# Kernel optimization log

Hardware: AMD Instinct MI355X
Metric: run time of the kernel (lower is better)

## Reference

```python
import jax, jax.numpy as jnp
import numpy as np


def setup_inputs() -> dict:
    key = jax.random.key(0)
    k0, k1, k2, k3, k4, k5 = jax.random.split(key, 6)
    B, H, P, L = 8, 128, 128, 4096
    u = jax.random.normal(k0, (B, H, L), dtype=jnp.float32)
    C2 = jax.random.normal(k1, (H, P, 2), dtype=jnp.float32)        # view_as_real(C)
    B_bar2 = jax.random.normal(k2, (P, H, 2), dtype=jnp.float32)    # view_as_real(B_bar)
    D = jax.random.normal(k3, (H, H), dtype=jnp.float32)
    # Frozen discrete diagonal state matrix: |lambda| in [strong, weak] = [0.9, 1.0]
    r = 0.9 + 0.1 * jax.random.uniform(k4, (P,), dtype=jnp.float32)
    th = 2.0 * jnp.pi * jax.random.uniform(k5, (P,), dtype=jnp.float32)
    Lambda_bar2 = jnp.stack([r * jnp.cos(th), r * jnp.sin(th)], axis=-1)
    return {"u": u, "C2": C2, "B_bar2": B_bar2, "D": D, "Lambda_bar2": Lambda_bar2}


def reference(u, C2, B_bar2, D, Lambda_bar2):
    L = u.shape[-1]
    Lam = Lambda_bar2[:, 0] + 1j * Lambda_bar2[:, 1]           # (P,)
    omega = 2.0 * jnp.pi * jnp.fft.rfftfreq(L).astype(jnp.float32)  # (Lf,)
    # Cauchy-like frequency kernel: 1 / (i*omega - Lambda)  -> (P, Lf)
    kernel = 1.0 / (1j * omega[None, :] - Lam[:, None])
    C = C2[..., 0] + 1j * C2[..., 1]                           # (H, P)
    B_bar = B_bar2[..., 0] + 1j * B_bar2[..., 1]               # (P, H)
    U_s = jnp.fft.rfftn(u)                                     # n-dim FFT (faithful to torch.fft.rfftn(u))
    C_kernel = jnp.einsum('hp,pl->hpl', C, kernel)             # (H, P, Lf)
    G = jnp.einsum('hpl,pq->hql', C_kernel, B_bar)             # (H, H, Lf)
    Y_s = jnp.einsum('hql,bql->bhl', G, U_s) + jnp.einsum('hq,bql->bhl', D.astype(U_s.dtype), U_s)
    y = jnp.fft.irfftn(Y_s)                                    # (B, H, L)
    return jax.nn.gelu(y, approximate=False)                   # torch nn.GELU default = exact erf
```

## Files before the change

### kernel.cpp

```cpp
#include <hip/hip_runtime.h>
#include <math.h>

#define PI_F 3.14159265358979323846f
#define NB 8
#define NH 128
#define NL 4096
#define LF 2049
#define WB 2064
#define NT 16512

typedef float2 cpx;
typedef __attribute__((ext_vector_type(8))) short bf8v;
typedef __attribute__((ext_vector_type(4))) float f4;

#define MFMA16(a, b, c) __builtin_amdgcn_mfma_f32_16x16x32_bf16(a, b, c, 0, 0, 0)

__device__ __forceinline__ float gelu_exact(float x) {
  return 0.5f * x * (1.0f + erff(x * 0.70710678118654752f));
}
__device__ __forceinline__ unsigned short f2bf(float f) {
  unsigned int x = __float_as_uint(f);
  return (unsigned short)((x + 0x7FFFu + ((x >> 16) & 1u)) >> 16);
}
__device__ __forceinline__ float bf2f(unsigned short h) {
  return __uint_as_float((unsigned int)h << 16);
}
__device__ __forceinline__ unsigned int packpair(float re, float im) {
  return (unsigned int)f2bf(re) | ((unsigned int)f2bf(im) << 16);
}
__device__ __forceinline__ cpx cadd(cpx a, cpx b) { return make_float2(a.x + b.x, a.y + b.y); }
__device__ __forceinline__ cpx csub(cpx a, cpx b) { return make_float2(a.x - b.x, a.y - b.y); }
__device__ __forceinline__ cpx cmul(cpx a, cpx b) {
  return make_float2(fmaf(a.x, b.x, -a.y * b.y), fmaf(a.x, b.y, a.y * b.x));
}
template <int SGN>
__device__ __forceinline__ cpx mulJ(cpx a) {
  return (SGN < 0) ? make_float2(a.y, -a.x) : make_float2(-a.y, a.x);
}

__global__ __launch_bounds__(128) void precomp_pack(
    const float* __restrict__ C2, const float* __restrict__ B2,
    const float* __restrict__ D,
    unsigned short* __restrict__ Mbh, unsigned short* __restrict__ Mbl,
    unsigned short* __restrict__ Mch, unsigned short* __restrict__ Mcl) {
  __shared__ float rc[128], rs[128];
  __shared__ float sTr[128], sTi[128];
  int x = blockIdx.x, t = threadIdx.x, which = blockIdx.y;
  { float s, c; sincosf(-(2.f * PI_F / 128.f) * (float)t, &s, &c); rc[t] = c; rs[t] = s; }
  __syncthreads();
  float sr = 0.f, si = 0.f;
  if (which == 0) {
    for (int k = 0; k < 128; ++k) {
      int j = (k * t) & 127; float c = rc[j], s = rs[j];
      float br = B2[(x * 128 + k) * 2], bi = B2[(x * 128 + k) * 2 + 1];
      sr += br * c - bi * s; si += br * s + bi * c;
    }
    auto wr = [&](int r, int c, float v) {
      unsigned short h = f2bf(v);
      Mbh[r * 256 + c] = h; Mbl[r * 256 + c] = f2bf(v - bf2f(h));
    };
    wr(2 * x,     2 * t,     sr);  wr(2 * x,     2 * t + 1, -si);
    wr(2 * x + 1, 2 * t,     si);  wr(2 * x + 1, 2 * t + 1,  sr);
  } else if (which == 1) {
    for (int k = 0; k < 128; ++k) {
      int j = (k * t) & 127; float c = rc[j], s = -rs[j];
      float cr = C2[(k * 128 + x) * 2], ci = C2[(k * 128 + x) * 2 + 1];
      sr += cr * c - ci * s; si += cr * s + ci * c;
    }
    sr *= (1.f / 128.f); si *= (1.f / 128.f);
    auto wr = [&](int r, int c, float v) {
      unsigned short h = f2bf(v);
      Mch[r * 512 + c] = h; Mcl[r * 512 + c] = f2bf(v - bf2f(h));
    };
    wr(2 * t,     2 * x,     sr);  wr(2 * t,     2 * x + 1, -si);
    wr(2 * t + 1, 2 * x,     si);  wr(2 * t + 1, 2 * x + 1,  sr);
  } else {
    for (int k = 0; k < 128; ++k) {
      int j = (k * x) & 127; float c = rc[j], s = rs[j];
      float d = D[t * 128 + k];
      sr += d * c; si += d * s;
    }
    sTr[t] = sr; sTi[t] = si;
    __syncthreads();
    sr = 0.f; si = 0.f;
    for (int k = 0; k < 128; ++k) {
      int j = (k * t) & 127; float c = rc[j], s = -rs[j];
      sr += sTr[k] * c - sTi[k] * s;
      si += sTr[k] * s + sTi[k] * c;
    }
    sr *= (1.f / 128.f); si *= (1.f / 128.f);
    auto wr = [&](int r, int c, float v) {
      unsigned short h = f2bf(v);
      Mch[r * 512 + c] = h; Mcl[r * 512 + c] = f2bf(v - bf2f(h));
    };
    wr(2 * t,     256 + 2 * x,     sr);  wr(2 * t,     256 + 2 * x + 1, -si);
    wr(2 * t + 1, 256 + 2 * x,     si);  wr(2 * t + 1, 256 + 2 * x + 1,  sr);
  }
}

#define SW(k) ((k) ^ (((k) >> 4) & 31))

template <int SGN>
__device__ __forceinline__ void dft8(cpx a[8]) {
  cpx t0 = cadd(a[0], a[4]), u0 = csub(a[0], a[4]);
  cpx t1 = cadd(a[1], a[5]), u1 = csub(a[1], a[5]);
  cpx t2 = cadd(a[2], a[6]), u2 = csub(a[2], a[6]);
  cpx t3 = cadd(a[3], a[7]), u3 = csub(a[3], a[7]);
  cpx E0 = cadd(t0, t2), E2 = csub(t0, t2);
  cpx ju2 = mulJ<SGN>(u2);
  cpx E1 = cadd(u0, ju2), E3 = csub(u0, ju2);
  cpx O0 = cadd(t1, t3), O2 = csub(t1, t3);
  cpx ju3 = mulJ<SGN>(u3);
  cpx O1 = cadd(u1, ju3), O3 = csub(u1, ju3);
  const float r = 0.70710678118654752f;
  const float S = (float)SGN;
  cpx w1O1 = make_float2(r * (O1.x - S * O1.y), r * (O1.y + S * O1.x));
  cpx w3O3 = make_float2(r * (-O3.x - S * O3.y), r * (S * O3.x - O3.y));
  cpx jO2 = mulJ<SGN>(O2);
  a[0] = cadd(E0, O0);   a[4] = csub(E0, O0);
  a[1] = cadd(E1, w1O1); a[5] = csub(E1, w1O1);
  a[2] = cadd(E2, jO2);  a[6] = csub(E2, jO2);
  a[3] = cadd(E3, w3O3); a[7] = csub(E3, w3O3);
}

template <int SGN>
__device__ __forceinline__ void dft4(cpx b[4]) {
  cpx s0 = cadd(b[0], b[2]), d0 = csub(b[0], b[2]);
  cpx s1 = cadd(b[1], b[3]), d1 = csub(b[1], b[3]);
  cpx jd1 = mulJ<SGN>(d1);
  b[0] = cadd(s0, s1); b[2] = csub(s0, s1);
  b[1] = cadd(d0, jd1); b[3] = csub(d0, jd1);
}

__device__ __forceinline__ void twid8(cpx a[8], float ang) {
  float s, c; __sincosf(ang, &s, &c);
  cpx w1 = make_float2(c, s);
  cpx w2 = cmul(w1, w1), w3 = cmul(w2, w1), w4 = cmul(w2, w2);
  cpx w5 = cmul(w3, w2), w6 = cmul(w3, w3), w7 = cmul(w4, w3);
  a[1] = cmul(a[1], w1); a[2] = cmul(a[2], w2); a[3] = cmul(a[3], w3);
  a[4] = cmul(a[4], w4); a[5] = cmul(a[5], w5); a[6] = cmul(a[6], w6);
  a[7] = cmul(a[7], w7);
}

template <int SGN>
__device__ __forceinline__ void fft2048_core(cpx a[8], cpx* __restrict__ bufA,
                                             cpx* __restrict__ bufB, int t) {
  const float S = (float)SGN;
  dft8<SGN>(a);
  twid8(a, S * (2.f * PI_F / 2048.f) * (float)t);
#pragma unroll
  for (int p = 0; p < 8; ++p) bufA[p * 264 + t] = a[p];
  __syncthreads();
  int p = t >> 5, n1 = t & 31;
#pragma unroll
  for (int j = 0; j < 8; ++j) a[j] = bufA[p * 264 + n1 + 32 * j];
  dft8<SGN>(a);
  twid8(a, S * (2.f * PI_F / 256.f) * (float)n1);
#pragma unroll
  for (int q = 0; q < 8; ++q) bufB[p * 264 + q * 33 + n1] = a[q];
  __syncthreads();
  int q = (t >> 2) & 7, n2 = t & 3;
#pragma unroll
  for (int j = 0; j < 8; ++j) a[j] = bufB[p * 264 + q * 33 + n2 + 4 * j];
  dft8<SGN>(a);
  twid8(a, S * (2.f * PI_F / 32.f) * (float)n2);
#pragma unroll
  for (int d = 0; d < 8; ++d) bufA[p * 264 + q * 33 + 4 * d + n2] = a[d];
  __syncthreads();
#pragma unroll
  for (int h = 0; h < 2; ++h) {
    int d = 2 * n2 + h;
    cpx b[4];
#pragma unroll
    for (int m = 0; m < 4; ++m) b[m] = bufA[p * 264 + q * 33 + 4 * d + m];
    dft4<SGN>(b);
    int kb = p + 8 * q + 64 * d;
#pragma unroll
    for (int c = 0; c < 4; ++c) bufB[SW(kb + 512 * c)] = b[c];
  }
  __syncthreads();
}

__global__ __launch_bounds__(256) void fft_fwd_pack(const float* __restrict__ u,
                                                    unsigned int* __restrict__ Uph) {
  __shared__ cpx bufA[2112], bufB[2112];
  int t = threadIdx.x;
  int row = blockIdx.x;
  int b = row >> 7, q = row & 127;
  const cpx* src = (const cpx*)(u + (size_t)row * NL);
  cpx a[8];
#pragma unroll
  for (int j = 0; j < 8; ++j) a[j] = src[t + 256 * j];
  fft2048_core<-1>(a, bufA, bufB, t);
  unsigned int* Uh = Uph + (size_t)q * NT + (size_t)b * WB;
  auto pstore = [&](int k, float ur, float ui) { Uh[k] = packpair(ur, ui); };
#pragma unroll
  for (int r = 0; r < 4; ++r) {
    int k = t + (r << 8);
    if (k == 0) {
      cpx z0 = bufB[SW(0)];
      pstore(0, z0.x + z0.y, 0.f);
      pstore(2048, z0.x - z0.y, 0.f);
      cpx zN = bufB[SW(1024)];
      pstore(1024, zN.x, -zN.y);
    } else {
      cpx A = bufB[SW(k)];
      cpx M = bufB[SW(2048 - k)];
      float Br = M.x, Bi = -M.y;
      float sr = 0.5f * (A.x + Br), si = 0.5f * (A.y + Bi);
      float dr = 0.5f * (A.x - Br), di = 0.5f * (A.y - Bi);
      float th = (float)k * (PI_F / 2048.f);
      float sn, cs; __sincosf(th, &sn, &cs);
      float tr = cs * dr + sn * di;
      float ti = cs * di - sn * dr;
      pstore(k, sr + ti, si - tr);
      float A2r = M.x, A2i = M.y;
      float B2r = A.x, B2i = -A.y;
      float s2r = 0.5f * (A2r + B2r), s2i = 0.5f * (A2i + B2i);
      float d2r = 0.5f * (A2r - B2r), d2i = 0.5f * (A2i - B2i);
      float t2r = -cs * d2r + sn * d2i;
      float t2i = -cs * d2i - sn * d2r;
      pstore(2048 - k, s2r + t2i, s2i - t2r);
    }
  }
}

__global__ __launch_bounds__(256, 2) void gemm_fused(
    const unsigned short* __restrict__ Mbh, const unsigned short* __restrict__ Mbl,
    const unsigned short* __restrict__ Mch, const unsigned short* __restrict__ Mcl,
    const unsigned int* __restrict__ Uph,
    const float* __restrict__ Lam,
    float2* __restrict__ Yp) {
  __shared__ unsigned short Ah[8192], Al[8192];
  __shared__ unsigned short Bh[2048];
  __shared__ unsigned int Vl[8192];
  int tid = threadIdx.x;
  int j0 = blockIdx.x * 64;
  int w = tid >> 6, lane = tid & 63, quad = lane >> 4, ln = lane & 15;
  int colB = tid & 63, grpB = tid >> 6;
  f4 acc[4][4];
#pragma unroll
  for (int mt = 0; mt < 4; ++mt)
#pragma unroll
    for (int nt = 0; nt < 4; ++nt) acc[mt][nt] = (f4){0.f, 0.f, 0.f, 0.f};

  for (int kt = 0; kt < 256; kt += 32) {
    __syncthreads();
#pragma unroll
    for (int r = 0; r < 4; ++r) {
      int j = tid + 256 * r; int m = j >> 2, cch = j & 3;
      int slot = (m * 4 + (cch ^ (m & 3))) * 8;
      size_t go = (size_t)m * 256 + kt + cch * 8;
      *(uint4*)&Ah[slot] = *(const uint4*)&Mbh[go];
      *(uint4*)&Al[slot] = *(const uint4*)&Mbl[go];
    }
    {
      size_t base = (size_t)((kt >> 1) + grpB * 4) * NT + j0 + colB;
      uint4 hv;
      hv.x = Uph[base];          hv.y = Uph[base + NT];
      hv.z = Uph[base + 2 * NT]; hv.w = Uph[base + 3 * NT];
      *(uint4*)&Bh[(grpB * 64 + colB) * 8] = hv;
    }
    __syncthreads();
    bf8v ah[4], al[4], bh[4];
#pragma unroll
    for (int mt = 0; mt < 4; ++mt) {
      int m = w * 64 + mt * 16 + ln;
      int off = (m * 4 + (quad ^ (m & 3))) * 8;
      ah[mt] = *(const bf8v*)&Ah[off];
      al[mt] = *(const bf8v*)&Al[off];
    }
#pragma unroll
    for (int nt = 0; nt < 4; ++nt)
      bh[nt] = *(const bf8v*)&Bh[(quad * 64 + nt * 16 + ln) * 8];
#pragma unroll
    for (int mt = 0; mt < 4; ++mt)
#pragma unroll
      for (int nt = 0; nt < 4; ++nt) {
        acc[mt][nt] = MFMA16(ah[mt], bh[nt], acc[mt][nt]);
        acc[mt][nt] = MFMA16(al[mt], bh[nt], acc[mt][nt]);
      }
  }
  __syncthreads();
#pragma unroll
  for (int mt = 0; mt < 4; ++mt) {
    int r0 = w * 64 + mt * 16 + quad * 4;
    int p0 = r0 >> 1;
    float2 lam0 = ((const float2*)Lam)[p0];
    float2 lam1 = ((const float2*)Lam)[p0 + 1];
#pragma unroll
    for (int nt = 0; nt < 4; ++nt) {
      int col = nt * 16 + ln;
      int gcol = j0 + col;
      int bb = gcol / WB; int l = gcol - bb * WB;
      float omega = (float)l * (PI_F / 2048.f);
      f4 a = acc[mt][nt];
      float dx0 = -lam0.x, dy0 = omega - lam0.y;
      float inv0 = 1.f / (dx0 * dx0 + dy0 * dy0);
      float kr0 = dx0 * inv0, ki0 = -dy0 * inv0;
      float v0r = kr0 * a[0] - ki0 * a[1];
      float v0i = kr0 * a[1] + ki0 * a[0];
      float dx1 = -lam1.x, dy1 = omega - lam1.y;
      float inv1 = 1.f / (dx1 * dx1 + dy1 * dy1);
      float kr1 = dx1 * inv1, ki1 = -dy1 * inv1;
      float v1r = kr1 * a[2] - ki1 * a[3];
      float v1i = kr1 * a[3] + ki1 * a[2];
      int gc = (p0 >> 2) * 64 + col;
      Vl[gc * 4 + (p0 & 3)] = packpair(v0r, v0i);
      Vl[gc * 4 + ((p0 + 1) & 3)] = packpair(v1r, v1i);
    }
  }
  __syncthreads();

#pragma unroll
  for (int mt = 0; mt < 4; ++mt)
#pragma unroll
    for (int nt = 0; nt < 4; ++nt) acc[mt][nt] = (f4){0.f, 0.f, 0.f, 0.f};
  const unsigned short* Vs = (const unsigned short*)Vl;
  for (int kt = 0; kt < 512; kt += 32) {
    __syncthreads();
#pragma unroll
    for (int r = 0; r < 4; ++r) {
      int j = tid + 256 * r; int m = j >> 2, cch = j & 3;
      int slot = (m * 4 + (cch ^ (m & 3))) * 8;
      size_t go = (size_t)m * 512 + kt + cch * 8;
      *(uint4*)&Ah[slot] = *(const uint4*)&Mch[go];
      *(uint4*)&Al[slot] = *(const uint4*)&Mcl[go];
    }
    if (kt >= 256) {
      size_t base = (size_t)(((kt - 256) >> 1) + grpB * 4) * NT + j0 + colB;
      uint4 hv;
      hv.x = Uph[base];          hv.y = Uph[base + NT];
      hv.z = Uph[base + 2 * NT]; hv.w = Uph[base + 3 * NT];
      *(uint4*)&Bh[(grpB * 64 + colB) * 8] = hv;
    }
    __syncthreads();
    bf8v ah[4], al[4], bh[4];
#pragma unroll
    for (int mt = 0; mt < 4; ++mt) {
      int m = w * 64 + mt * 16 + ln;
      int off = (m * 4 + (quad ^ (m & 3))) * 8;
      ah[mt] = *(const bf8v*)&Ah[off];
      al[mt] = *(const bf8v*)&Al[off];
    }
    if (kt < 256) {
#pragma unroll
      for (int nt = 0; nt < 4; ++nt)
        bh[nt] = *(const bf8v*)&Vs[(((kt >> 3) + quad) * 64 + nt * 16 + ln) * 8];
    } else {
#pragma unroll
      for (int nt = 0; nt < 4; ++nt)
        bh[nt] = *(const bf8v*)&Bh[(quad * 64 + nt * 16 + ln) * 8];
    }
#pragma unroll
    for (int mt = 0; mt < 4; ++mt)
#pragma unroll
      for (int nt = 0; nt < 4; ++nt) {
        acc[mt][nt] = MFMA16(ah[mt], bh[nt], acc[mt][nt]);
        acc[mt][nt] = MFMA16(al[mt], bh[nt], acc[mt][nt]);
      }
  }
#pragma unroll
  for (int mt = 0; mt < 4; ++mt) {
    int r0 = w * 64 + mt * 16 + quad * 4;
    int h0 = r0 >> 1;
#pragma unroll
    for (int nt = 0; nt < 4; ++nt) {
      int gcol = j0 + nt * 16 + ln;
      f4 a = acc[mt][nt];
      Yp[(size_t)h0 * NT + gcol] = make_float2(a[0], a[1]);
      Yp[(size_t)(h0 + 1) * NT + gcol] = make_float2(a[2], a[3]);
    }
  }
}

__global__ __launch_bounds__(256) void fft_inv_gelu_pl(const float2* __restrict__ Yp,
                                                       float* __restrict__ out) {
  __shared__ cpx bufA[2112], bufB[2112];
  int t = threadIdx.x;
  int row = blockIdx.x;
  int b = row >> 7, h = row & 127;
  const float2* Yrow = Yp + (size_t)h * NT + (size_t)b * WB;
#pragma unroll
  for (int r = 0; r < 4; ++r) {
    int k = t + (r << 8);
    if (k == 0) {
      float y0 = Yrow[0].x;
      float yN = Yrow[2048].x;
      bufB[SW(0)] = make_float2(0.5f * (y0 + yN), 0.5f * (y0 - yN));
      float2 z = Yrow[1024];
      bufB[SW(1024)] = make_float2(z.x, -z.y);
    } else {
      float2 A = Yrow[k];
      float2 M = Yrow[2048 - k];
      float Br = M.x, Bi = -M.y;
      float sr = 0.5f * (A.x + Br), si = 0.5f * (A.y + Bi);
      float dr = 0.5f * (A.x - Br), di = 0.5f * (A.y - Bi);
      float th = (float)k * (PI_F / 2048.f);
      float sn, cs; __sincosf(th, &sn, &cs);
      float e1 = cs * di + sn * dr;
      float e2 = cs * dr - sn * di;
      bufB[SW(k)] = make_float2(sr - e1, si + e2);
      bufB[SW(2048 - k)] = make_float2(sr + e1, -si + e2);
    }
  }
  __syncthreads();
  cpx a[8];
#pragma unroll
  for (int j = 0; j < 8; ++j) a[j] = bufB[SW(t + 256 * j)];
  fft2048_core<1>(a, bufA, bufB, t);
  float2* dst = (float2*)(out + (size_t)row * NL);
  const float sc = 1.f / 2048.f;
#pragma unroll
  for (int r = 0; r < 8; ++r) {
    int n = t + (r << 8);
    cpx z = bufB[SW(n)];
    dst[n] = make_float2(gelu_exact(z.x * sc), gelu_exact(z.y * sc));
  }
}

__global__ __launch_bounds__(128) void fb_precomp(
    const float* __restrict__ C2, const float* __restrict__ B2,
    const float* __restrict__ D,
    float* __restrict__ Bt, float* __restrict__ Ct, float* __restrict__ Dt) {
  __shared__ float rc[128], rs[128];
  __shared__ float sTr[128], sTi[128];
  int x = blockIdx.x, t = threadIdx.x, which = blockIdx.y;
  { float s, c; sincosf(-(2.f * PI_F / 128.f) * (float)t, &s, &c); rc[t] = c; rs[t] = s; }
  __syncthreads();
  float sr = 0.f, si = 0.f;
  if (which == 0) {
    for (int k = 0; k < 128; ++k) {
      int j = (k * t) & 127; float c = rc[j], s = rs[j];
      float br = B2[(x * 128 + k) * 2], bi = B2[(x * 128 + k) * 2 + 1];
      sr += br * c - bi * s; si += br * s + bi * c;
    }
    Bt[(t * 128 + x) * 2] = sr; Bt[(t * 128 + x) * 2 + 1] = si;
  } else if (which == 1) {
    for (int k = 0; k < 128; ++k) {
      int j = (k * t) & 127; float c = rc[j], s = -rs[j];
      float cr = C2[(k * 128 + x) * 2], ci = C2[(k * 128 + x) * 2 + 1];
      sr += cr * c - ci * s; si += cr * s + ci * c;
    }
    Ct[(x * 128 + t) * 2] = sr * (1.f / 128.f);
    Ct[(x * 128 + t) * 2 + 1] = si * (1.f / 128.f);
  } else {
    for (int k = 0; k < 128; ++k) {
      int j = (k * x) & 127; float c = rc[j], s = rs[j];
      float d = D[t * 128 + k];
      sr += d * c; si += d * s;
    }
    sTr[t] = sr; sTi[t] = si;
    __syncthreads();
    sr = 0.f; si = 0.f;
    for (int k = 0; k < 128; ++k) {
      int j = (k * t) & 127; float c = rc[j], s = -rs[j];
      sr += sTr[k] * c - sTi[k] * s;
      si += sTr[k] * s + sTi[k] * c;
    }
    Dt[(x * 128 + t) * 2] = sr * (1.f / 128.f);
    Dt[(x * 128 + t) * 2 + 1] = si * (1.f / 128.f);
  }
}

__global__ __launch_bounds__(256) void fb_fft_fwd(const float* __restrict__ u,
                                                  cpx* __restrict__ U) {
  __shared__ cpx bufA[2112], bufB[2112];
  int t = threadIdx.x;
  int row = blockIdx.x;
  const cpx* src = (const cpx*)(u + (size_t)row * NL);
  cpx a[8];
#pragma unroll
  for (int j = 0; j < 8; ++j) a[j] = src[t + 256 * j];
  fft2048_core<-1>(a, bufA, bufB, t);
  cpx* Urow = U + (size_t)row * LF;
#pragma unroll
  for (int r = 0; r < 4; ++r) {
    int k = t + (r << 8);
    if (k == 0) {
      cpx z0 = bufB[SW(0)];
      Urow[0] = make_float2(z0.x + z0.y, 0.f);
      Urow[2048] = make_float2(z0.x - z0.y, 0.f);
      cpx zN = bufB[SW(1024)];
      Urow[1024] = make_float2(zN.x, -zN.y);
    } else {
      cpx A = bufB[SW(k)];
      cpx M = bufB[SW(2048 - k)];
      float Br = M.x, Bi = -M.y;
      float sr = 0.5f * (A.x + Br), si = 0.5f * (A.y + Bi);
      float dr = 0.5f * (A.x - Br), di = 0.5f * (A.y - Bi);
      float th = (float)k * (PI_F / 2048.f);
      float sn, cs; __sincosf(th, &sn, &cs);
      float tr = cs * dr + sn * di;
      float ti = cs * di - sn * dr;
      Urow[k] = make_float2(sr + ti, si - tr);
      float A2r = M.x, A2i = M.y;
      float B2r = A.x, B2i = -A.y;
      float s2r = 0.5f * (A2r + B2r), s2i = 0.5f * (A2i + B2i);
      float d2r = 0.5f * (A2r - B2r), d2i = 0.5f * (A2i - B2i);
      float t2r = -cs * d2r + sn * d2i;
      float t2i = -cs * d2i - sn * d2r;
      Urow[2048 - k] = make_float2(s2r + t2i, s2i - t2r);
    }
  }
}

__device__ __forceinline__ void ld4(float4 d[4], const float4* __restrict__ p) {
#pragma unroll
  for (int kk = 0; kk < 4; ++kk) d[kk] = p[kk];
}
__device__ __forceinline__ void cmac4(const float4 m[4], float xr, float xi,
                                      float ar[8], float ai[8]) {
#pragma unroll
  for (int kk = 0; kk < 4; ++kk) {
    float4 v = m[kk];
    ar[2 * kk]     = fmaf(v.x, xr, fmaf(-v.y, xi, ar[2 * kk]));
    ai[2 * kk]     = fmaf(v.x, xi, fmaf( v.y, xr, ai[2 * kk]));
    ar[2 * kk + 1] = fmaf(v.z, xr, fmaf(-v.w, xi, ar[2 * kk + 1]));
    ai[2 * kk + 1] = fmaf(v.z, xi, fmaf( v.w, xr, ai[2 * kk + 1]));
  }
}

__global__ __launch_bounds__(256) void fb_mix(
    const cpx* __restrict__ U,
    const float* __restrict__ Bt, const float* __restrict__ Ct,
    const float* __restrict__ Dt, const float* __restrict__ Lam,
    cpx* __restrict__ Y) {
  __shared__ cpx sU[128][17], sV[128][17];
  int tid = threadIdx.x;
  int b = blockIdx.y;
  size_t ub = (size_t)b * NH * LF;
  if (blockIdx.x == 128) {
    int t = tid;
    if (t < 128) sU[t][0] = U[ub + (size_t)t * LF + 2048];
    __syncthreads();
    if (t < 128) {
      float ar = 0.f, ai = 0.f;
      for (int q = 0; q < 128; ++q) {
        float ur = sU[q][0].x, ui = sU[q][0].y;
        float br = Bt[(q * 128 + t) * 2], bi = Bt[(q * 128 + t) * 2 + 1];
        ar = fmaf(br, ur, fmaf(-bi, ui, ar));
        ai = fmaf(br, ui, fmaf(bi, ur, ai));
      }
      float a = Lam[2 * t], bb = Lam[2 * t + 1];
      float dx = -a, dy = PI_F - bb;
      float inv = 1.f / (dx * dx + dy * dy);
      float kr = dx * inv, ki = -dy * inv;
      sV[t][0] = make_float2(kr * ar - ki * ai, kr * ai + ki * ar);
    }
    __syncthreads();
    if (t < 128) {
      float ar = 0.f, ai = 0.f;
      for (int q = 0; q < 128; ++q) {
        float ur = sU[q][0].x, ui = sU[q][0].y;
        float vr = sV[q][0].x, vi = sV[q][0].y;
        float cr = Ct[(q * 128 + t) * 2], ci = Ct[(q * 128 + t) * 2 + 1];
        float dr = Dt[(q * 128 + t) * 2], di = Dt[(q * 128 + t) * 2 + 1];
        ar += cr * vr - ci * vi + dr * ur - di * ui;
        ai += cr * vi + ci * vr + dr * ui + di * ur;
      }
      Y[ub + (size_t)t * LF + 2048] = make_float2(ar, ai);
    }
    return;
  }
  int lane = tid & 15, g = tid >> 4;
  int l = blockIdx.x * 16 + lane;
#pragma unroll
  for (int rep = 0; rep < 8; ++rep) {
    int q = rep * 16 + g;
    sU[q][lane] = U[ub + (size_t)q * LF + l];
  }
  __syncthreads();
  float omega = (float)l * (PI_F / 2048.f);
  float ar[8], ai[8];
  {
#pragma unroll
    for (int k = 0; k < 8; ++k) { ar[k] = 0.f; ai[k] = 0.f; }
    const float4* base = (const float4*)Bt + g * 4;
    float4 e[4], o[4];
    ld4(e, base);
#pragma unroll 1
    for (int q = 0; q < 128; q += 2) {
      ld4(o, base + (q + 1) * 64);
      cpx u0 = sU[q][lane];
      cmac4(e, u0.x, u0.y, ar, ai);
      ld4(e, base + ((q + 2) & 127) * 64);
      cpx u1 = sU[q + 1][lane];
      cmac4(o, u1.x, u1.y, ar, ai);
    }
    int p0 = g * 8;
#pragma unroll
    for (int k = 0; k < 8; ++k) {
      int p = p0 + k;
      float a = Lam[2 * p], bb = Lam[2 * p + 1];
      float dx = -a, dy = omega - bb;
      float inv = 1.f / (dx * dx + dy * dy);
      float kr = dx * inv, ki = -dy * inv;
      sV[p][lane] = make_float2(kr * ar[k] - ki * ai[k], kr * ai[k] + ki * ar[k]);
    }
  }
  __syncthreads();
  {
#pragma unroll
    for (int k = 0; k < 8; ++k) { ar[k] = 0.f; ai[k] = 0.f; }
    const float4* base = (const float4*)Ct + g * 4;
    float4 e[4], o[4];
    ld4(e, base);
#pragma unroll 1
    for (int q = 0; q < 128; q += 2) {
      ld4(o, base + (q + 1) * 64);
      cpx v0 = sV[q][lane];
      cmac4(e, v0.x, v0.y, ar, ai);
      ld4(e, base + ((q + 2) & 127) * 64);
      cpx v1 = sV[q + 1][lane];
      cmac4(o, v1.x, v1.y, ar, ai);
    }
  }
  {
    const float4* base = (const float4*)Dt + g * 4;
    float4 e[4], o[4];
    ld4(e, base);
#pragma unroll 1
    for (int q = 0; q < 128; q += 2) {
      ld4(o, base + (q + 1) * 64);
      cpx u0 = sU[q][lane];
      cmac4(e, u0.x, u0.y, ar, ai);
      ld4(e, base + ((q + 2) & 127) * 64);
      cpx u1 = sU[q + 1][lane];
      cmac4(o, u1.x, u1.y, ar, ai);
    }
  }
  int h0 = g * 8;
#pragma unroll
  for (int k = 0; k < 8; ++k) {
    Y[ub + (size_t)(h0 + k) * LF + l] = make_float2(ar[k], ai[k]);
  }
}

__global__ __launch_bounds__(256) void fb_fft_inv(const cpx* __restrict__ Y,
                                                  float* __restrict__ out) {
  __shared__ cpx bufA[2112], bufB[2112];
  int t = threadIdx.x;
  int row = blockIdx.x;
  const cpx* Yrow = Y + (size_t)row * LF;
#pragma unroll
  for (int r = 0; r < 4; ++r) {
    int k = t + (r << 8);
    if (k == 0) {
      float y0 = Yrow[0].x;
      float yN = Yrow[2048].x;
      bufB[SW(0)] = make_float2(0.5f * (y0 + yN), 0.5f * (y0 - yN));
      cpx z = Yrow[1024];
      bufB[SW(1024)] = make_float2(z.x, -z.y);
    } else {
      cpx A = Yrow[k];
      cpx M = Yrow[2048 - k];
      float Br = M.x, Bi = -M.y;
      float sr = 0.5f * (A.x + Br), si = 0.5f * (A.y + Bi);
      float dr = 0.5f * (A.x - Br), di = 0.5f * (A.y - Bi);
      float th = (float)k * (PI_F / 2048.f);
      float sn, cs; __sincosf(th, &sn, &cs);
      float e1 = cs * di + sn * dr;
      float e2 = cs * dr - sn * di;
      bufB[SW(k)] = make_float2(sr - e1, si + e2);
      bufB[SW(2048 - k)] = make_float2(sr + e1, -si + e2);
    }
  }
  __syncthreads();
  cpx a[8];
#pragma unroll
  for (int j = 0; j < 8; ++j) a[j] = bufB[SW(t + 256 * j)];
  fft2048_core<1>(a, bufA, bufB, t);
  float2* dst = (float2*)(out + (size_t)row * NL);
  const float sc = 1.f / 2048.f;
#pragma unroll
  for (int r = 0; r < 8; ++r) {
    int n = t + (r << 8);
    cpx z = bufB[SW(n)];
    dst[n] = make_float2(gelu_exact(z.x * sc), gelu_exact(z.y * sc));
  }
}

extern "C" void kernel_launch(void* const* d_in, const int* in_sizes, int n_in,
                              void* d_out, int out_size, void* d_ws, size_t ws_size,
                              hipStream_t stream) {
  const float* u   = (const float*)d_in[0];
  const float* C2  = (const float*)d_in[1];
  const float* B2  = (const float*)d_in[2];
  const float* D   = (const float*)d_in[3];
  const float* Lam = (const float*)d_in[4];
  float* out = (float*)d_out;

  const size_t PL = (size_t)128 * NT;
  const size_t need = PL * 4
                    + PL * 8
                    + 2 * 65536 * 2 + 2 * 131072 * 2;

  if (ws_size >= need) {
    unsigned int* Uph = (unsigned int*)d_ws;
    float2* Yp = (float2*)(Uph + PL);
    unsigned short* Mbh = (unsigned short*)(Yp + PL);
    unsigned short* Mbl = Mbh + 65536;
    unsigned short* Mch = Mbl + 65536;
    unsigned short* Mcl = Mch + 131072;

    precomp_pack<<<dim3(128, 3), 128, 0, stream>>>(C2, B2, D, Mbh, Mbl, Mch, Mcl);
    fft_fwd_pack<<<NB * NH, 256, 0, stream>>>(u, Uph);
    gemm_fused<<<NT / 64, 256, 0, stream>>>(Mbh, Mbl, Mch, Mcl, Uph, Lam, Yp);
    fft_inv_gelu_pl<<<NB * NH, 256, 0, stream>>>(Yp, out);
  } else {
    float* ws = (float*)d_ws;
    const size_t nUc = (size_t)NB * NH * LF;
    cpx* U  = (cpx*)ws;
    cpx* Yf = U;
    float* Bt = ws + 2 * nUc;
    float* Ct = Bt + 32768;
    float* Dt = Ct + 32768;
    fb_precomp<<<dim3(128, 3), 128, 0, stream>>>(C2, B2, D, Bt, Ct, Dt);
    fb_fft_fwd<<<NB * NH, 256, 0, stream>>>(u, U);
    fb_mix<<<dim3(129, NB), 256, 0, stream>>>(U, Bt, Ct, Dt, Lam, Yf);
    fb_fft_inv<<<NB * NH, 256, 0, stream>>>(Yf, out);
  }
}
```

Baseline: 150.9 us.

## Pipeline GEMM with async LDS loads and merge precompute into forward FFT launch

The two stages of the mixing GEMM now use double-buffered LDS with direct global-to-LDS loads (global_load_lds) on pre-tiled, pre-swizzled weight matrices. The B operand is prefetched into registers one tile ahead, and explicit vmcnt waits replace the per-tile __syncthreads. The precompute kernel is folded into the forward FFT launch as extra blocks, removing one launch. The GEMM occupancy hint drops to one block per CU, and the V buffer is padded to avoid bank conflicts. The manual waitcnt-based synchronization across waves is fragile.

```diff
diff --git a/kernel.cpp b/kernel.cpp
--- a/kernel.cpp
+++ b/kernel.cpp
@@ -38,64 +38,20 @@
   return (SGN < 0) ? make_float2(a.y, -a.x) : make_float2(-a.y, a.x);
 }
 
-__global__ __launch_bounds__(128) void precomp_pack(
-    const float* __restrict__ C2, const float* __restrict__ B2,
-    const float* __restrict__ D,
-    unsigned short* __restrict__ Mbh, unsigned short* __restrict__ Mbl,
-    unsigned short* __restrict__ Mch, unsigned short* __restrict__ Mcl) {
-  __shared__ float rc[128], rs[128];
-  __shared__ float sTr[128], sTi[128];
-  int x = blockIdx.x, t = threadIdx.x, which = blockIdx.y;
-  { float s, c; sincosf(-(2.f * PI_F / 128.f) * (float)t, &s, &c); rc[t] = c; rs[t] = s; }
-  __syncthreads();
-  float sr = 0.f, si = 0.f;
-  if (which == 0) {
-    for (int k = 0; k < 128; ++k) {
-      int j = (k * t) & 127; float c = rc[j], s = rs[j];
-      float br = B2[(x * 128 + k) * 2], bi = B2[(x * 128 + k) * 2 + 1];
-      sr += br * c - bi * s; si += br * s + bi * c;
-    }
-    auto wr = [&](int r, int c, float v) {
-      unsigned short h = f2bf(v);
-      Mbh[r * 256 + c] = h; Mbl[r * 256 + c] = f2bf(v - bf2f(h));
-    };
-    wr(2 * x,     2 * t,     sr);  wr(2 * x,     2 * t + 1, -si);
-    wr(2 * x + 1, 2 * t,     si);  wr(2 * x + 1, 2 * t + 1,  sr);
-  } else if (which == 1) {
-    for (int k = 0; k < 128; ++k) {
-      int j = (k * t) & 127; float c = rc[j], s = -rs[j];
-      float cr = C2[(k * 128 + x) * 2], ci = C2[(k * 128 + x) * 2 + 1];
-      sr += cr * c - ci * s; si += cr * s + ci * c;
-    }
-    sr *= (1.f / 128.f); si *= (1.f / 128.f);
-    auto wr = [&](int r, int c, float v) {
-      unsigned short h = f2bf(v);
-      Mch[r * 512 + c] = h; Mcl[r * 512 + c] = f2bf(v - bf2f(h));
-    };
-    wr(2 * t,     2 * x,     sr);  wr(2 * t,     2 * x + 1, -si);
-    wr(2 * t + 1, 2 * x,     si);  wr(2 * t + 1, 2 * x + 1,  sr);
-  } else {
-    for (int k = 0; k < 128; ++k) {
-      int j = (k * x) & 127; float c = rc[j], s = rs[j];
-      float d = D[t * 128 + k];
-      sr += d * c; si += d * s;
-    }
-    sTr[t] = sr; sTi[t] = si;
-    __syncthreads();
-    sr = 0.f; si = 0.f;
-    for (int k = 0; k < 128; ++k) {
-      int j = (k * t) & 127; float c = rc[j], s = -rs[j];
-      sr += sTr[k] * c - sTi[k] * s;
-      si += sTr[k] * s + sTi[k] * c;
-    }
-    sr *= (1.f / 128.f); si *= (1.f / 128.f);
-    auto wr = [&](int r, int c, float v) {
-      unsigned short h = f2bf(v);
-      Mch[r * 512 + c] = h; Mcl[r * 512 + c] = f2bf(v - bf2f(h));
-    };
-    wr(2 * t,     256 + 2 * x,     sr);  wr(2 * t,     256 + 2 * x + 1, -si);
-    wr(2 * t + 1, 256 + 2 * x,     si);  wr(2 * t + 1, 256 + 2 * x + 1,  sr);
-  }
+__device__ __forceinline__ void wrM(unsigned short* __restrict__ H,
+                                    unsigned short* __restrict__ L,
+                                    int m, int k, float v) {
+  size_t a = (size_t)(k >> 5) * 8192 +
+             (size_t)(m * 4 + (((k >> 3) & 3) ^ (m & 3))) * 8 + (k & 7);
+  unsigned short h = f2bf(v);
+  H[a] = h;
+  L[a] = f2bf(v - bf2f(h));
+}
+
+__device__ __forceinline__ void gload16(const unsigned short* g, unsigned short* l) {
+  __builtin_amdgcn_global_load_lds(
+      (const __attribute__((address_space(1))) unsigned int*)g,
+      (__attribute__((address_space(3))) unsigned int*)l, 16, 0, 0);
 }
 
 #define SW(k) ((k) ^ (((k) >> 4) & 31))
@@ -181,11 +137,69 @@
   __syncthreads();
 }
 
-__global__ __launch_bounds__(256) void fft_fwd_pack(const float* __restrict__ u,
-                                                    unsigned int* __restrict__ Uph) {
+__global__ __launch_bounds__(256) void fwd_pre(
+    const float* __restrict__ u,
+    const float* __restrict__ C2, const float* __restrict__ B2,
+    const float* __restrict__ D,
+    unsigned int* __restrict__ Uph,
+    unsigned short* __restrict__ Mbh, unsigned short* __restrict__ Mbl,
+    unsigned short* __restrict__ Mch, unsigned short* __restrict__ Mcl) {
   __shared__ cpx bufA[2112], bufB[2112];
   int t = threadIdx.x;
-  int row = blockIdx.x;
+  if (blockIdx.x < 192) {
+    __shared__ float rc[128], rs[128];
+    __shared__ float sTr[2][128], sTi[2][128];
+    int e = blockIdx.x;
+    int which = e >> 6;
+    int half = t >> 7, tt = t & 127;
+    int x = (2 * e + half) & 127;
+    { float s, c; sincosf(-(2.f * PI_F / 128.f) * (float)tt, &s, &c); rc[tt] = c; rs[tt] = s; }
+    __syncthreads();
+    float sr = 0.f, si = 0.f;
+    if (which == 0) {
+      for (int k = 0; k < 128; ++k) {
+        int j = (k * tt) & 127; float c = rc[j], s = rs[j];
+        float br = B2[(x * 128 + k) * 2], bi = B2[(x * 128 + k) * 2 + 1];
+        sr += br * c - bi * s; si += br * s + bi * c;
+      }
+      wrM(Mbh, Mbl, 2 * x,     2 * tt,     sr);
+      wrM(Mbh, Mbl, 2 * x,     2 * tt + 1, -si);
+      wrM(Mbh, Mbl, 2 * x + 1, 2 * tt,     si);
+      wrM(Mbh, Mbl, 2 * x + 1, 2 * tt + 1,  sr);
+    } else if (which == 1) {
+      for (int k = 0; k < 128; ++k) {
+        int j = (k * tt) & 127; float c = rc[j], s = -rs[j];
+        float cr = C2[(k * 128 + x) * 2], ci = C2[(k * 128 + x) * 2 + 1];
+        sr += cr * c - ci * s; si += cr * s + ci * c;
+      }
+      sr *= (1.f / 128.f); si *= (1.f / 128.f);
+      wrM(Mch, Mcl, 2 * tt,     2 * x,     sr);
+      wrM(Mch, Mcl, 2 * tt,     2 * x + 1, -si);
+      wrM(Mch, Mcl, 2 * tt + 1, 2 * x,     si);
+      wrM(Mch, Mcl, 2 * tt + 1, 2 * x + 1,  sr);
+    } else {
+      for (int k = 0; k < 128; ++k) {
+        int j = (k * x) & 127; float c = rc[j], s = rs[j];
+        float d = D[tt * 128 + k];
+        sr += d * c; si += d * s;
+      }
+      sTr[half][tt] = sr; sTi[half][tt] = si;
+      __syncthreads();
+      sr = 0.f; si = 0.f;
+      for (int k = 0; k < 128; ++k) {
+        int j = (k * tt) & 127; float c = rc[j], s = -rs[j];
+        sr += sTr[half][k] * c - sTi[half][k] * s;
+        si += sTr[half][k] * s + sTi[half][k] * c;
+      }
+      sr *= (1.f / 128.f); si *= (1.f / 128.f);
+      wrM(Mch, Mcl, 2 * tt,     256 + 2 * x,     sr);
+      wrM(Mch, Mcl, 2 * tt,     256 + 2 * x + 1, -si);
+      wrM(Mch, Mcl, 2 * tt + 1, 256 + 2 * x,     si);
+      wrM(Mch, Mcl, 2 * tt + 1, 256 + 2 * x + 1,  sr);
+    }
+    return;
+  }
+  int row = blockIdx.x - 192;
   int b = row >> 7, q = row & 127;
   const cpx* src = (const cpx*)(u + (size_t)row * NL);
   cpx a[8];
@@ -225,54 +239,64 @@
   }
 }
 
-__global__ __launch_bounds__(256, 2) void gemm_fused(
+__global__ __launch_bounds__(256, 1) void gemm_fused(
     const unsigned short* __restrict__ Mbh, const unsigned short* __restrict__ Mbl,
     const unsigned short* __restrict__ Mch, const unsigned short* __restrict__ Mcl,
     const unsigned int* __restrict__ Uph,
     const float* __restrict__ Lam,
     float2* __restrict__ Yp) {
-  __shared__ unsigned short Ah[8192], Al[8192];
-  __shared__ unsigned short Bh[2048];
-  __shared__ unsigned int Vl[8192];
+  __shared__ unsigned short Ah[2][8192], Al[2][8192];
+  __shared__ unsigned int Vl[8448];
   int tid = threadIdx.x;
   int j0 = blockIdx.x * 64;
   int w = tid >> 6, lane = tid & 63, quad = lane >> 4, ln = lane & 15;
-  int colB = tid & 63, grpB = tid >> 6;
+
+  unsigned int breg[2][4][4];
   f4 acc[4][4];
-#pragma unroll
-  for (int mt = 0; mt < 4; ++mt)
-#pragma unroll
-    for (int nt = 0; nt < 4; ++nt) acc[mt][nt] = (f4){0.f, 0.f, 0.f, 0.f};
-
-  for (int kt = 0; kt < 256; kt += 32) {
-    __syncthreads();
-#pragma unroll
-    for (int r = 0; r < 4; ++r) {
-      int j = tid + 256 * r; int m = j >> 2, cch = j & 3;
-      int slot = (m * 4 + (cch ^ (m & 3))) * 8;
-      size_t go = (size_t)m * 256 + kt + cch * 8;
-      *(uint4*)&Ah[slot] = *(const uint4*)&Mbh[go];
-      *(uint4*)&Al[slot] = *(const uint4*)&Mbl[go];
-    }
-    {
-      size_t base = (size_t)((kt >> 1) + grpB * 4) * NT + j0 + colB;
-      uint4 hv;
-      hv.x = Uph[base];          hv.y = Uph[base + NT];
-      hv.z = Uph[base + 2 * NT]; hv.w = Uph[base + 3 * NT];
-      *(uint4*)&Bh[(grpB * 64 + colB) * 8] = hv;
-    }
-    __syncthreads();
-    bf8v ah[4], al[4], bh[4];
+
+#define STAGE_A(H, L, tile, buf)                                              \
+  {                                                                           \
+    size_t tb_ = (size_t)(tile) * 8192;                                       \
+    _Pragma("unroll") for (int r_ = 0; r_ < 4; ++r_) {                        \
+      int sb_ = w * 256 + r_ * 64;                                            \
+      gload16((H) + tb_ + (size_t)(sb_ + lane) * 8, &Ah[buf][sb_ * 8]);       \
+      gload16((L) + tb_ + (size_t)(sb_ + lane) * 8, &Al[buf][sb_ * 8]);       \
+    }                                                                         \
+  }
+#define LOAD_B(g, it)                                                         \
+  {                                                                           \
+    _Pragma("unroll") for (int nt_ = 0; nt_ < 4; ++nt_)                       \
+      _Pragma("unroll") for (int c_ = 0; c_ < 4; ++c_)                        \
+        breg[g][nt_][c_] =                                                    \
+            Uph[(size_t)((it) * 16 + quad * 4 + c_) * NT + j0 + nt_ * 16 + ln]; \
+  }
+#define VMW(n) asm volatile("s_waitcnt vmcnt(" #n ")" ::: "memory")
+#define LGW()  asm volatile("s_waitcnt lgkmcnt(0)" ::: "memory")
+
+  auto bFromReg = [&](int g, bf8v bh[4]) {
+#pragma unroll
+    for (int nt = 0; nt < 4; ++nt) {
+      union { unsigned int u[4]; bf8v v; } cv;
+#pragma unroll
+      for (int c = 0; c < 4; ++c) cv.u[c] = breg[g][nt][c];
+      bh[nt] = cv.v;
+    }
+  };
+  auto bFromV = [&](int i, bf8v bh[4]) {
+    const unsigned short* Vs = (const unsigned short*)Vl;
+#pragma unroll
+    for (int nt = 0; nt < 4; ++nt)
+      bh[nt] = *(const bf8v*)&Vs[(size_t)(i * 4 + quad) * 528 + (nt * 16 + ln) * 8];
+  };
+  auto compute = [&](int buf, const bf8v* bh) {
+    bf8v ah[4], al[4];
 #pragma unroll
     for (int mt = 0; mt < 4; ++mt) {
       int m = w * 64 + mt * 16 + ln;
       int off = (m * 4 + (quad ^ (m & 3))) * 8;
-      ah[mt] = *(const bf8v*)&Ah[off];
-      al[mt] = *(const bf8v*)&Al[off];
-    }
-#pragma unroll
-    for (int nt = 0; nt < 4; ++nt)
-      bh[nt] = *(const bf8v*)&Bh[(quad * 64 + nt * 16 + ln) * 8];
+      ah[mt] = *(const bf8v*)&Ah[buf][off];
+      al[mt] = *(const bf8v*)&Al[buf][off];
+    }
 #pragma unroll
     for (int mt = 0; mt < 4; ++mt)
 #pragma unroll
@@ -280,8 +304,30 @@
         acc[mt][nt] = MFMA16(ah[mt], bh[nt], acc[mt][nt]);
         acc[mt][nt] = MFMA16(al[mt], bh[nt], acc[mt][nt]);
       }
-  }
-  __syncthreads();
+  };
+
+  STAGE_A(Mbh, Mbl, 0, 0);
+  LOAD_B(0, 0);
+#pragma unroll
+  for (int mt = 0; mt < 4; ++mt)
+#pragma unroll
+    for (int nt = 0; nt < 4; ++nt) acc[mt][nt] = (f4){0.f, 0.f, 0.f, 0.f};
+
+#pragma unroll
+  for (int i = 0; i < 8; ++i) {
+    LGW();
+    if (i < 7) {
+      STAGE_A(Mbh, Mbl, i + 1, (i + 1) & 1);
+      LOAD_B((i + 1) & 1, i + 1);
+      VMW(24);
+    } else {
+      VMW(0);
+    }
+    bf8v bh[4];
+    bFromReg(i & 1, bh);
+    compute(i & 1, bh);
+  }
+
 #pragma unroll
   for (int mt = 0; mt < 4; ++mt) {
     int r0 = w * 64 + mt * 16 + quad * 4;
@@ -305,61 +351,49 @@
       float kr1 = dx1 * inv1, ki1 = -dy1 * inv1;
       float v1r = kr1 * a[2] - ki1 * a[3];
       float v1i = kr1 * a[3] + ki1 * a[2];
-      int gc = (p0 >> 2) * 64 + col;
-      Vl[gc * 4 + (p0 & 3)] = packpair(v0r, v0i);
-      Vl[gc * 4 + ((p0 + 1) & 3)] = packpair(v1r, v1i);
-    }
-  }
-  __syncthreads();
-
+      int ch = p0 >> 2;
+      Vl[ch * 264 + col * 4 + (p0 & 3)] = packpair(v0r, v0i);
+      Vl[ch * 264 + col * 4 + ((p0 + 1) & 3)] = packpair(v1r, v1i);
+    }
+  }
+  __syncthreads();
+
+  STAGE_A(Mch, Mcl, 0, 0);
 #pragma unroll
   for (int mt = 0; mt < 4; ++mt)
 #pragma unroll
     for (int nt = 0; nt < 4; ++nt) acc[mt][nt] = (f4){0.f, 0.f, 0.f, 0.f};
-  const unsigned short* Vs = (const unsigned short*)Vl;
-  for (int kt = 0; kt < 512; kt += 32) {
-    __syncthreads();
-#pragma unroll
-    for (int r = 0; r < 4; ++r) {
-      int j = tid + 256 * r; int m = j >> 2, cch = j & 3;
-      int slot = (m * 4 + (cch ^ (m & 3))) * 8;
-      size_t go = (size_t)m * 512 + kt + cch * 8;
-      *(uint4*)&Ah[slot] = *(const uint4*)&Mch[go];
-      *(uint4*)&Al[slot] = *(const uint4*)&Mcl[go];
-    }
-    if (kt >= 256) {
-      size_t base = (size_t)(((kt - 256) >> 1) + grpB * 4) * NT + j0 + colB;
-      uint4 hv;
-      hv.x = Uph[base];          hv.y = Uph[base + NT];
-      hv.z = Uph[base + 2 * NT]; hv.w = Uph[base + 3 * NT];
-      *(uint4*)&Bh[(grpB * 64 + colB) * 8] = hv;
-    }
-    __syncthreads();
-    bf8v ah[4], al[4], bh[4];
-#pragma unroll
-    for (int mt = 0; mt < 4; ++mt) {
-      int m = w * 64 + mt * 16 + ln;
-      int off = (m * 4 + (quad ^ (m & 3))) * 8;
-      ah[mt] = *(const bf8v*)&Ah[off];
-      al[mt] = *(const bf8v*)&Al[off];
-    }
-    if (kt < 256) {
-#pragma unroll
-      for (int nt = 0; nt < 4; ++nt)
-        bh[nt] = *(const bf8v*)&Vs[(((kt >> 3) + quad) * 64 + nt * 16 + ln) * 8];
+
+#pragma unroll
+  for (int i = 0; i < 8; ++i) {
+    LGW();
+    if (i < 7) {
+      STAGE_A(Mch, Mcl, i + 1, (i + 1) & 1);
+      VMW(8);
     } else {
-#pragma unroll
-      for (int nt = 0; nt < 4; ++nt)
-        bh[nt] = *(const bf8v*)&Bh[(quad * 64 + nt * 16 + ln) * 8];
-    }
-#pragma unroll
-    for (int mt = 0; mt < 4; ++mt)
-#pragma unroll
-      for (int nt = 0; nt < 4; ++nt) {
-        acc[mt][nt] = MFMA16(ah[mt], bh[nt], acc[mt][nt]);
-        acc[mt][nt] = MFMA16(al[mt], bh[nt], acc[mt][nt]);
-      }
-  }
+      STAGE_A(Mch, Mcl, 8, 0);
+      LOAD_B(0, 0);
+      VMW(24);
+    }
+    bf8v bh[4];
+    bFromV(i, bh);
+    compute(i & 1, bh);
+  }
+#pragma unroll
+  for (int i = 8; i < 16; ++i) {
+    LGW();
+    if (i < 15) {
+      STAGE_A(Mch, Mcl, i + 1, (i + 1) & 1);
+      LOAD_B((i + 1) & 1, i + 1 - 8);
+      VMW(24);
+    } else {
+      VMW(0);
+    }
+    bf8v bh[4];
+    bFromReg(i & 1, bh);
+    compute(i & 1, bh);
+  }
+
 #pragma unroll
   for (int mt = 0; mt < 4; ++mt) {
     int r0 = w * 64 + mt * 16 + quad * 4;
@@ -372,6 +406,10 @@
       Yp[(size_t)(h0 + 1) * NT + gcol] = make_float2(a[2], a[3]);
     }
   }
+#undef STAGE_A
+#undef LOAD_B
+#undef VMW
+#undef LGW
 }
 
 __global__ __launch_bounds__(256) void fft_inv_gelu_pl(const float2* __restrict__ Yp,
@@ -704,8 +742,7 @@
     unsigned short* Mch = Mbl + 65536;
     unsigned short* Mcl = Mch + 131072;
 
-    precomp_pack<<<dim3(128, 3), 128, 0, stream>>>(C2, B2, D, Mbh, Mbl, Mch, Mcl);
-    fft_fwd_pack<<<NB * NH, 256, 0, stream>>>(u, Uph);
+    fwd_pre<<<192 + NB * NH, 256, 0, stream>>>(u, C2, B2, D, Uph, Mbh, Mbl, Mch, Mcl);
     gemm_fused<<<NT / 64, 256, 0, stream>>>(Mbh, Mbl, Mch, Mcl, Uph, Lam, Yp);
     fft_inv_gelu_pl<<<NB * NH, 256, 0, stream>>>(Yp, out);
   } else {
```

Result: faster. 139.7 us (-7.4%).
